# Optimization experiments

Measured on AMD Instinct MI355X. Metric: run time of the kernel, lower is better.

The kernel has to match this reference:

```python
import jax, jax.numpy as jnp
import numpy as np

B, LO, LQ = 4, 2048, 2048
NIN, H, G, NH = 41, 128, 10, 2


def _lin(key, din, dout):
    kw, kb = jax.random.split(key)
    W = jax.random.normal(kw, (din, dout), jnp.float32) / np.float32(np.sqrt(din))
    b = jax.random.normal(kb, (dout,), jnp.float32) * 0.01
    return W, b


def setup_inputs() -> dict:
    key = jax.random.key(0)
    ks = jax.random.split(key, 24)
    t_obs = jax.random.normal(ks[0], (B, LO, 1), jnp.float32)
    ch_obs = jax.random.randint(ks[1], (B, LO, 1), 0, NIN).astype(jnp.float32)
    v_obs = jax.random.normal(ks[2], (B, LO, 1), jnp.float32)
    obs = jnp.concatenate([t_obs, ch_obs, v_obs], -1)  # [B, LO, 3]
    t_q = jax.random.normal(ks[3], (B, LQ, 1), jnp.float32)
    ch_q = jax.random.randint(ks[4], (B, LQ, 1), 0, NIN).astype(jnp.float32)
    xq = jnp.concatenate([t_q, ch_q], -1)  # [B, LQ, 2]
    mobs = (jax.random.uniform(ks[5], (B, LO)) < 0.9).astype(jnp.float32)
    mq = (jax.random.uniform(ks[6], (B, LQ)) < 0.9).astype(jnp.float32)
    w_q0, b_q0 = _lin(ks[7], 1, 1)
    w_q1, b_q1 = _lin(ks[8], 1, H - 1)
    w_o0, b_o0 = _lin(ks[9], 1, 1)
    w_o1, b_o1 = _lin(ks[10], 1, H - 1)
    w_cobs, b_cobs = _lin(ks[11], NIN, H)
    w_cq, b_cq = _lin(ks[12], NIN, H)
    w_qp, b_qp = _lin(ks[13], 2 * H, H)
    w_kp, b_kp = _lin(ks[14], 2 * H + 1, H)
    ws_q, ws_qb = _lin(ks[15], H, H * NH)
    ws_o, ws_ob = _lin(ks[16], H * NH, H)
    ww_q, ww_qb = _lin(ks[17], H, H * NH)
    ww_o, ww_ob = _lin(ks[18], H * NH, H)
    wc_q, wc_qb = _lin(ks[19], H, H * NH)
    wc_o, wc_ob = _lin(ks[20], H * NH, H)
    w_split, b_split = _lin(ks[21], H, H * G)
    mix_wt = jax.random.normal(ks[22], (G, H), jnp.float32)
    w_mix, b_mix = _lin(ks[23], H, 1)
    return dict(obs=obs, mobs=mobs, xq=xq, mq=mq,
                w_q0=w_q0, b_q0=b_q0, w_q1=w_q1, b_q1=b_q1,
                w_o0=w_o0, b_o0=b_o0, w_o1=w_o1, b_o1=b_o1,
                w_cobs=w_cobs, b_cobs=b_cobs, w_cq=w_cq, b_cq=b_cq,
                w_qp=w_qp, b_qp=b_qp, w_kp=w_kp, b_kp=b_kp,
                ws_q=ws_q, ws_qb=ws_qb, ws_o=ws_o, ws_ob=ws_ob,
                ww_q=ww_q, ww_qb=ww_qb, ww_o=ww_o, ww_ob=ww_ob,
                wc_q=wc_q, wc_qb=wc_qb, wc_o=wc_o, wc_ob=wc_ob,
                w_split=w_split, b_split=b_split,
                mix_wt=mix_wt, w_mix=w_mix, b_mix=b_mix)


def _mha(q_in, k_in, v_in, mask, Wq, bq, Wo, bo):
    # Faithful to original: query_param projects q, k AND v (key/val params are unused).
    Bb, Lq, _ = q_in.shape
    Lk = k_in.shape[1]
    q = (q_in @ Wq + bq).reshape(Bb, Lq, NH, H)
    k = (k_in @ Wq + bq).reshape(Bb, Lk, NH, H)
    v = (v_in @ Wq + bq).reshape(Bb, Lk, NH, H)
    scores = jnp.einsum('bqhd,bkhd->bhqk', q, k) / np.float32(np.sqrt(H))
    scores = jnp.where(mask[:, None, :, :] == 0, jnp.float32(-1e6), scores)
    attn = jax.nn.softmax(scores, axis=-1)
    out = jnp.einsum('bhqk,bkhd->bqhd', attn, v).reshape(Bb, Lq, NH * H)
    return q_in + out @ Wo + bo


def _forward(obs, mobs, xq, mq,
             w_q0, b_q0, w_q1, b_q1, w_o0, b_o0, w_o1, b_o1,
             w_cobs, b_cobs, w_cq, b_cq, w_qp, b_qp, w_kp, b_kp,
             ws_q, ws_qb, ws_o, ws_ob, ww_q, ww_qb, ww_o, ww_ob,
             wc_q, wc_qb, wc_o, wc_ob, w_split, b_split,
             mix_wt, w_mix, b_mix):
    cq = xq[:, :, 1]
    tq = xq[:, :, 0:1]
    cobs = obs[:, :, 1]
    tobs = obs[:, :, 0:1]
    xobs = obs[:, :, 2:]
    tq = jnp.concatenate([tq @ w_q0 + b_q0, jnp.sin(tq @ w_q1 + b_q1)], -1)        # [B, LQ, H]
    tobs = jnp.concatenate([tobs @ w_o0 + b_o0, jnp.sin(tobs @ w_o1 + b_o1)], -1)  # [B, LO, H]
    cobs = jax.nn.one_hot(cobs.astype(jnp.int32), NIN, dtype=obs.dtype)
    cq = jax.nn.one_hot(cq.astype(jnp.int32), NIN, dtype=obs.dtype)
    cobs = jax.nn.relu(cobs @ w_cobs + b_cobs)
    cq = jax.nn.relu(cq @ w_cq + b_cq)
    obs_ = jnp.concatenate([tobs, cobs, xobs], -1) * mobs[:, :, None]  # [B, LO, 2H+1]
    xq_ = jnp.concatenate([tq, cq], -1) * mq[:, :, None]               # [B, LQ, 2H]
    qry_embed = xq_ @ w_qp + b_qp    # [B, LQ, H]
    obs_embed = obs_ @ w_kp + b_kp   # [B, LO, H]
    mask_self = mobs[:, :, None] * mobs[:, None, :]   # [B, LO, LO]
    mask_cross = mq[:, :, None] * mobs[:, None, :]    # [B, LQ, LO]
    mask_wts = jnp.broadcast_to(mobs[:, None, :], (obs.shape[0], G, mobs.shape[1]))  # [B, G, LO]
    wts_query = jnp.broadcast_to(mix_wt[None], (obs.shape[0], G, H))
    x = jax.nn.relu(_mha(obs_embed, obs_embed, obs_embed, mask_self, ws_q, ws_qb, ws_o, ws_ob))
    mw_ = _mha(wts_query, x, x, mask_wts, ww_q, ww_qb, ww_o, ww_ob)
    mw = jax.nn.softmax((mw_ @ w_mix + b_mix)[..., 0], axis=-1)  # [B, G]
    x = jax.nn.relu(_mha(qry_embed, x, x, mask_cross, wc_q, wc_qb, wc_o, wc_ob))
    x = (x @ w_split + b_split).reshape(x.shape[0], x.shape[1], G, H)
    return jnp.transpose(x, (0, 2, 1, 3)), mw  # ([B, G, LQ, H], [B, G])


def reference(obs, mobs, xq, mq,
              w_q0, b_q0, w_q1, b_q1, w_o0, b_o0, w_o1, b_o1,
              w_cobs, b_cobs, w_cq, b_cq, w_qp, b_qp, w_kp, b_kp,
              ws_q, ws_qb, ws_o, ws_ob, ww_q, ww_qb, ww_o, ww_ob,
              wc_q, wc_qb, wc_o, wc_ob, w_split, b_split,
              mix_wt, w_mix, b_mix):
    return _forward(obs, mobs, xq, mq,
                    w_q0, b_q0, w_q1, b_q1, w_o0, b_o0, w_o1, b_o1,
                    w_cobs, b_cobs, w_cq, b_cq, w_qp, b_qp, w_kp, b_kp,
                    ws_q, ws_qb, ws_o, ws_ob, ww_q, ww_qb, ww_o, ww_ob,
                    wc_q, wc_qb, wc_o, wc_ob, w_split, b_split,
                    mix_wt, w_mix, b_mix)
```

## Files before the change

kernel.cpp:

```cpp
#include <hip/hip_runtime.h>
#include <hip/hip_bf16.h>

#define B_  4
#define L_  2048
#define H_  128
#define NH_ 2
#define G_  10
#define NIN_ 41

typedef __hip_bfloat16 bf16;
typedef __attribute__((ext_vector_type(8))) short bf16x8s;
typedef __attribute__((ext_vector_type(4))) float f32x4;

__device__ __forceinline__ unsigned short f2bf_bits(float x) {
    __hip_bfloat16 h = __float2bfloat16(x);
    return *reinterpret_cast<unsigned short*>(&h);
}
__device__ __forceinline__ float us2f(unsigned short s) {
    return __uint_as_float(((unsigned int)s) << 16);
}

__global__ __launch_bounds__(128)
void featq_kernel(const float* __restrict__ xq, const float* __restrict__ mq,
                  const float* __restrict__ w_q0, const float* __restrict__ b_q0,
                  const float* __restrict__ w_q1, const float* __restrict__ b_q1,
                  const float* __restrict__ w_cq, const float* __restrict__ b_cq,
                  bf16* __restrict__ featq)
{
    const int row = blockIdx.x;
    const int j   = threadIdx.x;
    const float t   = xq[row * 2 + 0];
    const float chf = xq[row * 2 + 1];
    int ch = (int)chf; ch = max(0, min(NIN_ - 1, ch));
    const float m   = mq[row];
    float tf;
    if (j == 0) tf = t * w_q0[0] + b_q0[0];
    else        tf = __sinf(t * w_q1[j - 1] + b_q1[j - 1]);
    float cf = fmaxf(w_cq[ch * H_ + j] + b_cq[j], 0.f);
    featq[(size_t)row * 256 + j]       = __float2bfloat16(tf * m);
    featq[(size_t)row * 256 + 128 + j] = __float2bfloat16(cf * m);
}

__global__ __launch_bounds__(128)
void feato_kernel(const float* __restrict__ obs, const float* __restrict__ mobs,
                  const float* __restrict__ w_o0, const float* __restrict__ b_o0,
                  const float* __restrict__ w_o1, const float* __restrict__ b_o1,
                  const float* __restrict__ w_cobs, const float* __restrict__ b_cobs,
                  bf16* __restrict__ feato)
{
    const int row = blockIdx.x;
    const int j   = threadIdx.x;
    const float t   = obs[row * 3 + 0];
    const float chf = obs[row * 3 + 1];
    const float xv  = obs[row * 3 + 2];
    int ch = (int)chf; ch = max(0, min(NIN_ - 1, ch));
    const float m   = mobs[row];
    float tf;
    if (j == 0) tf = t * w_o0[0] + b_o0[0];
    else        tf = __sinf(t * w_o1[j - 1] + b_o1[j - 1]);
    float cf = fmaxf(w_cobs[ch * H_ + j] + b_cobs[j], 0.f);
    bf16* r = feato + (size_t)row * 288;
    r[j]       = __float2bfloat16(tf * m);
    r[128 + j] = __float2bfloat16(cf * m);
    if (j == 0) r[256] = __float2bfloat16(xv * m);
    if (j < 31) r[257 + j] = __float2bfloat16(0.f);
}

struct WtArgs {
    const float* W[8];
    bf16* T[8];
    int K[8], Kp[8], N[8];
};
__global__ __launch_bounds__(288)
void wtrans_all_kernel(WtArgs a)
{
    const int i = blockIdx.y, n = blockIdx.x, k = threadIdx.x;
    if (n >= a.N[i] || k >= a.Kp[i]) return;
    a.T[i][(size_t)n * a.Kp[i] + k] =
        (k < a.K[i]) ? __float2bfloat16(a.W[i][(size_t)k * a.N[i] + n])
                     : __float2bfloat16(0.f);
}

__global__ __launch_bounds__(256)
void kvtrans_kernel(const bf16* __restrict__ in, bf16* __restrict__ out)
{
    __shared__ unsigned short tile[64 * 136];
    const int tid = threadIdx.x;
    const int l0 = blockIdx.x * 64;
    const int bh = blockIdx.y;
    const unsigned short* src = (const unsigned short*)(in + (size_t)bh * L_ * H_);
    unsigned short* dst = (unsigned short*)(out + (size_t)bh * H_ * L_);
    #pragma unroll
    for (int p = 0; p < 4; p++) {
        const int l = p * 16 + (tid >> 4);
        const int d0 = (tid & 15) * 8;
        *(uint4*)&tile[l * 136 + d0] = *(const uint4*)&src[(size_t)(l0 + l) * H_ + d0];
    }
    __syncthreads();
// ... 27 lines not shown
        bf16x8s af = *(const bf16x8s*)(arow + kc + quad * 8);
        #pragma unroll
        for (int c = 0; c < 4; c++) {
            bf16x8s wf = *(const bf16x8s*)(WT + (size_t)(n0 + c * 16 + l15) * K + kc + quad * 8);
            acc[c] = __builtin_amdgcn_mfma_f32_16x16x32_bf16(af, wf, acc[c], 0, 0, 0);
        }
    }

    #pragma unroll
    for (int c = 0; c < 4; c++) {
        const int n = n0 + c * 16 + l15;
        const float bv = bias[n];
        #pragma unroll
        for (int r = 0; r < 4; r++) {
            const int m = m0 + quad * 4 + r;
            float v = acc[c][r] + bv;
            if (R != nullptr) v += __bfloat162float(R[(size_t)m * N + n]);
            if (do_relu) v = fmaxf(v, 0.f);
            if (mode == 0) {
                ((float*)out)[(size_t)m * N + n] = v;
            } else if (mode == 1) {
                ((bf16*)out)[(size_t)m * N + n] = __float2bfloat16(v);
            } else if (mode == 2) {
                const int b = m >> 11, l = m & 2047, hh = n >> 7, d = n & 127;
                ((bf16*)out)[(((size_t)(b * NH_ + hh)) * L_ + l) * H_ + d] = __float2bfloat16(v);
            } else {
                const int b = m >> 11, q = m & 2047, g = n >> 7, hh = n & 127;
                ((float*)out)[(((size_t)(b * G_ + g)) * L_ + q) * H_ + hh] = v;
            }
        }
    }
}

#define KT_S 136
#define VT_S 72
#define PS_S 72

__global__ __launch_bounds__(512, 2)
void flash_attn_kernel(const bf16* __restrict__ Qb, const bf16* __restrict__ KVb,
                       const bf16* __restrict__ KVTb,
                       const float* __restrict__ mQ, const float* __restrict__ mK,
                       bf16* __restrict__ O)
{
    __shared__ __align__(16) char smem[90112];
    unsigned short* Ks = (unsigned short*)smem;
    unsigned short* Vs = (unsigned short*)(smem + 34816);
    unsigned short* Ps = (unsigned short*)(smem + 71680);
    float* Ocomb = (float*)smem;
    float* mcomb = (float*)(smem + 33792);
    float* lcomb = (float*)(smem + 34048);

    const int tid  = threadIdx.x;
    const int lane = tid & 63;
    const int wave = tid >> 6;
    const int half = wave >> 2;
    const int wq   = wave & 3;
    const int quad = lane >> 4;
    const int l15  = lane & 15;
    const int t256 = tid & 255;
    const int bh = blockIdx.x, b = bh >> 1, h = bh & 1;
    const int q0 = blockIdx.y * 64;

    const bf16* kvb = KVb  + (size_t)bh * L_ * H_;
    const bf16* kvt = KVTb + (size_t)bh * H_ * L_;
    const float* mkb = mK + b * L_;

    const bf16* qrow = Qb + ((size_t)bh * L_ + q0 + wq * 16 + l15) * H_;
    bf16x8s qf[4];
    #pragma unroll
    for (int kc = 0; kc < 4; kc++)
        qf[kc] = *(const bf16x8s*)(qrow + kc * 32 + quad * 8);

    bool qz[4];
    #pragma unroll
    for (int r = 0; r < 4; r++)
        qz[r] = (mQ != nullptr) && (mQ[b * L_ + q0 + wq * 16 + quad * 4 + r] == 0.f);

    float mo[4], li[4];
    f32x4 Oacc[8];
    #pragma unroll
    for (int r = 0; r < 4; r++) { mo[r] = -1e30f; li[r] = 0.f; }
    #pragma unroll
    for (int c = 0; c < 8; c++) Oacc[c] = (f32x4){0.f, 0.f, 0.f, 0.f};

    const float SCALE = 0.08838834764831845f;
    unsigned short* KsH = Ks + half * 64 * KT_S;
    unsigned short* VsH = Vs + half * 128 * VT_S;
    unsigned short* pw  = Ps + wave * 16 * PS_S;

    const int krow_b = t256 >> 4, kcol = (t256 & 15) * 8;
    const int vrow_b = t256 >> 3, vcol = (t256 & 7) * 8;

    uint4 rk[4], rv[4];
    const int ks0 = half * 1024;

    {
        const int kb = ks0;
        #pragma unroll
        for (int p = 0; p < 4; p++)
            rk[p] = *(const uint4*)(kvb + (size_t)(kb + p * 16 + krow_b) * H_ + kcol);
        #pragma unroll
        for (int p = 0; p < 4; p++)
            rv[p] = *(const uint4*)(kvt + (size_t)(p * 32 + vrow_b) * L_ + kb + vcol);
        #pragma unroll
        for (int p = 0; p < 4; p++)
            *(uint4*)&KsH[(p * 16 + krow_b) * KT_S + kcol] = rk[p];
        #pragma unroll
        for (int p = 0; p < 4; p++)
            *(uint4*)&VsH[(p * 32 + vrow_b) * VT_S + vcol] = rv[p];
    }
    __syncthreads();

    for (int it = 0; it < 16; it++) {
        const int kb = ks0 + it * 64;

        if (it + 1 < 16) {
            const int kn = kb + 64;
            #pragma unroll
            for (int p = 0; p < 4; p++)
                rk[p] = *(const uint4*)(kvb + (size_t)(kn + p * 16 + krow_b) * H_ + kcol);
            #pragma unroll
            for (int p = 0; p < 4; p++)
                rv[p] = *(const uint4*)(kvt + (size_t)(p * 32 + vrow_b) * L_ + kn + vcol);
        }

        float koff[4];
        #pragma unroll
        for (int t = 0; t < 4; t++)
            koff[t] = (mkb[kb + t * 16 + l15] != 0.f) ? 0.f : -1000000.f;

        f32x4 sa[4];
        #pragma unroll
        for (int t = 0; t < 4; t++) sa[t] = (f32x4){0.f, 0.f, 0.f, 0.f};
        #pragma unroll
        for (int t = 0; t < 4; t++)
            #pragma unroll
            for (int kc = 0; kc < 4; kc++) {
                bf16x8s kf = *(const bf16x8s*)&KsH[(t * 16 + l15) * KT_S + kc * 32 + quad * 8];
                sa[t] = __builtin_amdgcn_mfma_f32_16x16x32_bf16(qf[kc], kf, sa[t], 0, 0, 0);
            }

        float s[4][4], mx[4];
        #pragma unroll
        for (int r = 0; r < 4; r++) {
            #pragma unroll
            for (int t = 0; t < 4; t++) {
                const float v = sa[t][r] * SCALE + koff[t];
                s[t][r] = qz[r] ? -1000000.f : v;
            }
            mx[r] = fmaxf(fmaxf(s[0][r], s[1][r]), fmaxf(s[2][r], s[3][r]));
        }
        #pragma unroll
        for (int off = 1; off < 16; off <<= 1)
            #pragma unroll
            for (int r = 0; r < 4; r++) mx[r] = fmaxf(mx[r], __shfl_xor(mx[r], off));

        float al[4], rs[4];
        #pragma unroll
        for (int r = 0; r < 4; r++) {
            const float mn = fmaxf(mo[r], mx[r]);
            al[r] = __expf(mo[r] - mn);
            mo[r] = mn;
            rs[r] = 0.f;
        }
        #pragma unroll
        for (int t = 0; t < 4; t++)
            #pragma unroll
            for (int r = 0; r < 4; r++) {
                const float p = __expf(s[t][r] - mo[r]);
                rs[r] += p;
                pw[(quad * 4 + r) * PS_S + t * 16 + l15] = f2bf_bits(p);
            }
        #pragma unroll
        for (int off = 1; off < 16; off <<= 1)
            #pragma unroll
            for (int r = 0; r < 4; r++) rs[r] += __shfl_xor(rs[r], off);
        #pragma unroll
        for (int r = 0; r < 4; r++) li[r] = li[r] * al[r] + rs[r];
        #pragma unroll
        for (int c = 0; c < 8; c++)
            #pragma unroll
            for (int r = 0; r < 4; r++) Oacc[c][r] *= al[r];

        bf16x8s pf0 = *(bf16x8s*)&pw[l15 * PS_S + quad * 8];
        bf16x8s pf1 = *(bf16x8s*)&pw[l15 * PS_S + 32 + quad * 8];

        #pragma unroll
        for (int c = 0; c < 8; c++) {
            bf16x8s v0 = *(const bf16x8s*)&VsH[(c * 16 + l15) * VT_S + quad * 8];
            bf16x8s v1 = *(const bf16x8s*)&VsH[(c * 16 + l15) * VT_S + 32 + quad * 8];
            Oacc[c] = __builtin_amdgcn_mfma_f32_16x16x32_bf16(pf0, v0, Oacc[c], 0, 0, 0);
            Oacc[c] = __builtin_amdgcn_mfma_f32_16x16x32_bf16(pf1, v1, Oacc[c], 0, 0, 0);
        }

        __syncthreads();
        if (it + 1 < 16) {
            #pragma unroll
            for (int p = 0; p < 4; p++)
                *(uint4*)&KsH[(p * 16 + krow_b) * KT_S + kcol] = rk[p];
            #pragma unroll
            for (int p = 0; p < 4; p++)
                *(uint4*)&VsH[(p * 32 + vrow_b) * VT_S + vcol] = rv[p];
            __syncthreads();
        }
    }

    if (half == 1) {
        #pragma unroll
        for (int c = 0; c < 8; c++)
            #pragma unroll
            for (int r = 0; r < 4; r++)
                Ocomb[(size_t)(wq * 16 + quad * 4 + r) * 132 + c * 16 + l15] = Oacc[c][r];
        if (l15 == 0) {
            #pragma unroll
            for (int r = 0; r < 4; r++) {
                mcomb[wq * 16 + quad * 4 + r] = mo[r];
                lcomb[wq * 16 + quad * 4 + r] = li[r];
            }
        }
    }
    __syncthreads();
    if (half == 0) {
        bf16* orow = O + ((size_t)b * L_ + q0 + wq * 16) * (NH_ * H_) + h * H_;
        #pragma unroll
        for (int r = 0; r < 4; r++) {
            const int row = quad * 4 + r;
            const float m1 = mcomb[wq * 16 + row];
            const float l1 = lcomb[wq * 16 + row];
            const float M  = fmaxf(mo[r], m1);
            const float a0 = __expf(mo[r] - M);
            const float a1 = __expf(m1 - M);
            const float inv = 1.f / (a0 * li[r] + a1 * l1);
            #pragma unroll
            for (int c = 0; c < 8; c++)
                orow[(size_t)row * (NH_ * H_) + c * 16 + l15] =
                    __float2bfloat16((a0 * Oacc[c][r] +
                                      a1 * Ocomb[(size_t)(wq * 16 + row) * 132 + c * 16 + l15]) * inv);
        }
    }
}

__global__ __launch_bounds__(256)
void qmwb_kernel(const float* __restrict__ mixwt, const float* __restrict__ W,
                 const float* __restrict__ bias, bf16* __restrict__ qmwb)
{
    const int g = blockIdx.x;
    const int c = threadIdx.x;
    const int h = c >> 7, d = c & 127;
    if (g >= G_) { qmwb[((size_t)h * 16 + g) * 128 + d] = __float2bfloat16(0.f); return; }
    __shared__ float xr[128];
    if (c < 128) xr[c] = mixwt[g * 128 + c];
    __syncthreads();
    float acc = bias[c];
    #pragma unroll 8
    for (int i = 0; i < 128; i++)
        acc += xr[i] * W[i * 256 + c];
    qmwb[((size_t)h * 16 + g) * 128 + d] = __float2bfloat16(acc);
}

__global__ __launch_bounds__(256)
void mwpartial_kernel(const bf16* __restrict__ qmwb, const bf16* __restrict__ kvmw,
                      const float* __restrict__ mK,
                      float* __restrict__ mwO, float* __restrict__ mwM,
                      float* __restrict__ mwL)
{
    __shared__ __align__(16) unsigned short Ks[128 * 136];
    __shared__ float Qs[10 * 128];
    __shared__ float sc[10 * 128];
    __shared__ float mst[10], lst[10];

// ... 203 lines not shown
    bf16* kvmw  = (bf16*)(ws + 20 * MB + 512 * KB);
    bf16* kvT   = (bf16*)(ws + 24 * MB + 512 * KB);
    char* wbase = ws + 28 * MB + 512 * KB;
    bf16* wqpT  = (bf16*)(wbase + 0);
    bf16* wkpT  = (bf16*)(wbase + 64 * KB);
    bf16* wsqT  = (bf16*)(wbase + 136 * KB);
    bf16* wsoT  = (bf16*)(wbase + 200 * KB);
    bf16* wwqT  = (bf16*)(wbase + 264 * KB);
    bf16* wcqT  = (bf16*)(wbase + 328 * KB);
    bf16* wcoT  = (bf16*)(wbase + 392 * KB);
    bf16* wsplT = (bf16*)(wbase + 456 * KB);
    bf16* qmwb  = (bf16*)(wbase + 776 * KB);
    float* mwO  = (float*)(wbase + 784 * KB);
    float* mwM  = (float*)(wbase + 1424 * KB);
    float* mwL  = (float*)(wbase + 1432 * KB);
    float* mwat = (float*)(wbase + 1440 * KB);
    float* mw_  = (float*)(wbase + 1480 * KB);
    bf16* kvbs  = featq;
    bf16* qcb   = featq;
    bf16* kvcb  = (bf16*)(ws + 4 * MB);
    bf16* abuf2 = abuf;

    WtArgs wa;
    wa.W[0]=w_qp;   wa.T[0]=wqpT;  wa.K[0]=256; wa.Kp[0]=256; wa.N[0]=128;
    wa.W[1]=w_kp;   wa.T[1]=wkpT;  wa.K[1]=257; wa.Kp[1]=288; wa.N[1]=128;
    wa.W[2]=ws_q;   wa.T[2]=wsqT;  wa.K[2]=128; wa.Kp[2]=128; wa.N[2]=256;
    wa.W[3]=ws_o;   wa.T[3]=wsoT;  wa.K[3]=256; wa.Kp[3]=256; wa.N[3]=128;
    wa.W[4]=ww_q;   wa.T[4]=wwqT;  wa.K[4]=128; wa.Kp[4]=128; wa.N[4]=256;
    wa.W[5]=wc_q;   wa.T[5]=wcqT;  wa.K[5]=128; wa.Kp[5]=128; wa.N[5]=256;
    wa.W[6]=wc_o;   wa.T[6]=wcoT;  wa.K[6]=256; wa.Kp[6]=256; wa.N[6]=128;
    wa.W[7]=w_split;wa.T[7]=wsplT; wa.K[7]=128; wa.Kp[7]=128; wa.N[7]=1280;
    wtrans_all_kernel<<<dim3(1280, 8), 288, 0, stream>>>(wa);

    featq_kernel<<<NROW, 128, 0, stream>>>(xq, mq, w_q0, b_q0, w_q1, b_q1,
                                           w_cq, b_cq, featq);
    feato_kernel<<<NROW, 128, 0, stream>>>(obs, mobs, w_o0, b_o0, w_o1, b_o1,
                                           w_cobs, b_cobs, feato);
    gemm_kernel<<<dim3(NROW/32, 2), 128, 0, stream>>>(featq, wqpT, b_qp, nullptr,
                                                      qe_bf, 256, 128, 1, 0);
    gemm_kernel<<<dim3(NROW/32, 2), 128, 0, stream>>>(feato, wkpT, b_kp, nullptr,
                                                      oe_bf, 288, 128, 1, 0);
    gemm_kernel<<<dim3(NROW/32, 4), 128, 0, stream>>>(oe_bf, wsqT, ws_qb, nullptr,
                                                      kvbs, 128, 256, 2, 0);
    kvtrans_kernel<<<dim3(L_/64, B_*NH_), 256, 0, stream>>>(kvbs, kvT);
    flash_attn_kernel<<<dim3(B_*NH_, L_/64), 512, 0, stream>>>(kvbs, kvbs, kvT,
                                                               nullptr, mobs, abuf);
    gemm_kernel<<<dim3(NROW/32, 2), 128, 0, stream>>>(abuf, wsoT, ws_ob, oe_bf,
                                                      x_bf, 256, 128, 1, 1);
    qmwb_kernel<<<16, 256, 0, stream>>>(mix_wt, ww_q, ww_qb, qmwb);
    gemm_kernel<<<dim3(NROW/32, 4), 128, 0, stream>>>(x_bf, wwqT, ww_qb, nullptr,
                                                      kvmw, 128, 256, 2, 0);
    mwpartial_kernel<<<dim3(16, NH_, B_), 256, 0, stream>>>(qmwb, kvmw, mobs,
                                                            mwO, mwM, mwL);
    mwcombine_kernel<<<B_ * G_, 256, 0, stream>>>(mwO, mwM, mwL, mwat);
    mwproj_kernel<<<B_ * G_, 128, 0, stream>>>(mwat, mix_wt, ww_o, ww_ob, mw_);
    mwfinal_kernel<<<B_, 64, 0, stream>>>(mw_, w_mix, b_mix,
                                          out + (size_t)B_ * G_ * L_ * H_);
    gemm_kernel<<<dim3(2*NROW/32, 4), 128, 0, stream>>>(qe_bf, wcqT, wc_qb, nullptr,
                                                        qcb, 128, 256, 2, 0);
    kvtrans_kernel<<<dim3(L_/64, B_*NH_), 256, 0, stream>>>(kvcb, kvT);
    flash_attn_kernel<<<dim3(B_*NH_, L_/64), 512, 0, stream>>>(qcb, kvcb, kvT,
                                                               mq, mobs, abuf2);
    gemm_kernel<<<dim3(NROW/32, 2), 128, 0, stream>>>(abuf2, wcoT, wc_ob, qe_bf,
                                                      x2_bf, 256, 128, 1, 1);
    gemm_kernel<<<dim3(NROW/32, 20), 128, 0, stream>>>(x2_bf, wsplT, b_split, nullptr,
                                                       out, 128, 1280, 3, 0);

    (void)in_sizes; (void)n_in; (void)out_size;
}
```

Measured before the change: 496.0 us.

## Split flash attention keys four ways with two query tiles per wave

The flash attention kernel now splits the key range into four quarters instead of two. Each wave processes two 16-row query tiles against a 32-key block, so each K/V fragment loaded from shared memory feeds two MFMAs. Partial results from the three non-leading quarters are merged through shared memory in a four-way softmax combine. Separately, the two feature-embedding kernels are merged into one launch. The cost is more shared memory (about 100KB per block), which may limit occupancy given launch bounds of 2 blocks, plus more registers.

```diff
diff --git a/kernel.cpp b/kernel.cpp
--- a/kernel.cpp
+++ b/kernel.cpp
@@ -21,49 +21,48 @@
 }
 
 __global__ __launch_bounds__(128)
-void featq_kernel(const float* __restrict__ xq, const float* __restrict__ mq,
-                  const float* __restrict__ w_q0, const float* __restrict__ b_q0,
-                  const float* __restrict__ w_q1, const float* __restrict__ b_q1,
-                  const float* __restrict__ w_cq, const float* __restrict__ b_cq,
-                  bf16* __restrict__ featq)
-{
-    const int row = blockIdx.x;
+void featall_kernel(const float* __restrict__ xq, const float* __restrict__ mq,
+                    const float* __restrict__ obs, const float* __restrict__ mobs,
+                    const float* __restrict__ w_q0, const float* __restrict__ b_q0,
+                    const float* __restrict__ w_q1, const float* __restrict__ b_q1,
+                    const float* __restrict__ w_cq, const float* __restrict__ b_cq,
+                    const float* __restrict__ w_o0, const float* __restrict__ b_o0,
+                    const float* __restrict__ w_o1, const float* __restrict__ b_o1,
+                    const float* __restrict__ w_cobs, const float* __restrict__ b_cobs,
+                    bf16* __restrict__ featq, bf16* __restrict__ feato)
+{
+    const int blk = blockIdx.x;
     const int j   = threadIdx.x;
-    const float t   = xq[row * 2 + 0];
-    const float chf = xq[row * 2 + 1];
-    int ch = (int)chf; ch = max(0, min(NIN_ - 1, ch));
-    const float m   = mq[row];
-    float tf;
-    if (j == 0) tf = t * w_q0[0] + b_q0[0];
-    else        tf = __sinf(t * w_q1[j - 1] + b_q1[j - 1]);
-    float cf = fmaxf(w_cq[ch * H_ + j] + b_cq[j], 0.f);
-    featq[(size_t)row * 256 + j]       = __float2bfloat16(tf * m);
-    featq[(size_t)row * 256 + 128 + j] = __float2bfloat16(cf * m);
-}
-
-__global__ __launch_bounds__(128)
-void feato_kernel(const float* __restrict__ obs, const float* __restrict__ mobs,
-                  const float* __restrict__ w_o0, const float* __restrict__ b_o0,
-                  const float* __restrict__ w_o1, const float* __restrict__ b_o1,
-                  const float* __restrict__ w_cobs, const float* __restrict__ b_cobs,
-                  bf16* __restrict__ feato)
-{
-    const int row = blockIdx.x;
-    const int j   = threadIdx.x;
-    const float t   = obs[row * 3 + 0];
-    const float chf = obs[row * 3 + 1];
-    const float xv  = obs[row * 3 + 2];
-    int ch = (int)chf; ch = max(0, min(NIN_ - 1, ch));
-    const float m   = mobs[row];
-    float tf;
-    if (j == 0) tf = t * w_o0[0] + b_o0[0];
-    else        tf = __sinf(t * w_o1[j - 1] + b_o1[j - 1]);
-    float cf = fmaxf(w_cobs[ch * H_ + j] + b_cobs[j], 0.f);
-    bf16* r = feato + (size_t)row * 288;
-    r[j]       = __float2bfloat16(tf * m);
-    r[128 + j] = __float2bfloat16(cf * m);
-    if (j == 0) r[256] = __float2bfloat16(xv * m);
-    if (j < 31) r[257 + j] = __float2bfloat16(0.f);
+    const int NROW = B_ * L_;
+    if (blk < NROW) {
+        const int row = blk;
+        const float t   = xq[row * 2 + 0];
+        const float chf = xq[row * 2 + 1];
+        int ch = (int)chf; ch = max(0, min(NIN_ - 1, ch));
+        const float m   = mq[row];
+        float tf;
+        if (j == 0) tf = t * w_q0[0] + b_q0[0];
+        else        tf = __sinf(t * w_q1[j - 1] + b_q1[j - 1]);
+        float cf = fmaxf(w_cq[ch * H_ + j] + b_cq[j], 0.f);
+        featq[(size_t)row * 256 + j]       = __float2bfloat16(tf * m);
+        featq[(size_t)row * 256 + 128 + j] = __float2bfloat16(cf * m);
+    } else {
+        const int row = blk - NROW;
+        const float t   = obs[row * 3 + 0];
+        const float chf = obs[row * 3 + 1];
+        const float xv  = obs[row * 3 + 2];
+        int ch = (int)chf; ch = max(0, min(NIN_ - 1, ch));
+        const float m   = mobs[row];
+        float tf;
+        if (j == 0) tf = t * w_o0[0] + b_o0[0];
+        else        tf = __sinf(t * w_o1[j - 1] + b_o1[j - 1]);
+        float cf = fmaxf(w_cobs[ch * H_ + j] + b_cobs[j], 0.f);
+        bf16* r = feato + (size_t)row * 288;
+        r[j]       = __float2bfloat16(tf * m);
+        r[128 + j] = __float2bfloat16(cf * m);
+        if (j == 0) r[256] = __float2bfloat16(xv * m);
+        if (j < 31) r[257 + j] = __float2bfloat16(0.f);
+    }
 }
 
 struct WtArgs {
@@ -158,8 +157,8 @@
 }
 
 #define KT_S 136
-#define VT_S 72
-#define PS_S 72
+#define VT_S 40
+#define PS_S 40
 
 __global__ __launch_bounds__(512, 2)
 void flash_attn_kernel(const bf16* __restrict__ Qb, const bf16* __restrict__ KVb,
@@ -167,200 +166,248 @@
                        const float* __restrict__ mQ, const float* __restrict__ mK,
                        bf16* __restrict__ O)
 {
-    __shared__ __align__(16) char smem[90112];
-    unsigned short* Ks = (unsigned short*)smem;
-    unsigned short* Vs = (unsigned short*)(smem + 34816);
-    unsigned short* Ps = (unsigned short*)(smem + 71680);
-    float* Ocomb = (float*)smem;
-    float* mcomb = (float*)(smem + 33792);
-    float* lcomb = (float*)(smem + 34048);
+    __shared__ __align__(16) char smem[102912];
 
     const int tid  = threadIdx.x;
     const int lane = tid & 63;
     const int wave = tid >> 6;
-    const int half = wave >> 2;
-    const int wq   = wave & 3;
+    const int qtr  = wave >> 1;
+    const int qw   = wave & 1;
     const int quad = lane >> 4;
     const int l15  = lane & 15;
-    const int t256 = tid & 255;
     const int bh = blockIdx.x, b = bh >> 1, h = bh & 1;
     const int q0 = blockIdx.y * 64;
+
+    unsigned short* KsQ = (unsigned short*)(smem + qtr * 8704);
+    unsigned short* VsQ = (unsigned short*)(smem + 34816 + qtr * 10240);
+    unsigned short* pw  = (unsigned short*)(smem + 75776 + wave * 2560);
+    float* Ocomb = (float*)smem;
+    float* mcomb = (float*)(smem + 101376);
+    float* lcomb = (float*)(smem + 102144);
 
     const bf16* kvb = KVb  + (size_t)bh * L_ * H_;
     const bf16* kvt = KVTb + (size_t)bh * H_ * L_;
     const float* mkb = mK + b * L_;
 
-    const bf16* qrow = Qb + ((size_t)bh * L_ + q0 + wq * 16 + l15) * H_;
-    bf16x8s qf[4];
+    bf16x8s qf[2][4];
     #pragma unroll
-    for (int kc = 0; kc < 4; kc++)
-        qf[kc] = *(const bf16x8s*)(qrow + kc * 32 + quad * 8);
-
-    bool qz[4];
+    for (int qt = 0; qt < 2; qt++) {
+        const bf16* qrow = Qb + ((size_t)bh * L_ + q0 + qw * 32 + qt * 16 + l15) * H_;
+        #pragma unroll
+        for (int kc = 0; kc < 4; kc++)
+            qf[qt][kc] = *(const bf16x8s*)(qrow + kc * 32 + quad * 8);
+    }
+
+    bool qz[2][4];
     #pragma unroll
-    for (int r = 0; r < 4; r++)
-        qz[r] = (mQ != nullptr) && (mQ[b * L_ + q0 + wq * 16 + quad * 4 + r] == 0.f);
-
-    float mo[4], li[4];
-    f32x4 Oacc[8];
+    for (int qt = 0; qt < 2; qt++)
+        #pragma unroll
+        for (int r = 0; r < 4; r++)
+            qz[qt][r] = (mQ != nullptr) &&
+                        (mQ[b * L_ + q0 + qw * 32 + qt * 16 + quad * 4 + r] == 0.f);
+
+    float mo[2][4], li[2][4];
+    f32x4 Oacc[2][8];
     #pragma unroll
-    for (int r = 0; r < 4; r++) { mo[r] = -1e30f; li[r] = 0.f; }
-    #pragma unroll
-    for (int c = 0; c < 8; c++) Oacc[c] = (f32x4){0.f, 0.f, 0.f, 0.f};
+    for (int qt = 0; qt < 2; qt++) {
+        #pragma unroll
+        for (int r = 0; r < 4; r++) { mo[qt][r] = -1e30f; li[qt][r] = 0.f; }
+        #pragma unroll
+        for (int c = 0; c < 8; c++) Oacc[qt][c] = (f32x4){0.f, 0.f, 0.f, 0.f};
+    }
 
     const float SCALE = 0.08838834764831845f;
-    unsigned short* KsH = Ks + half * 64 * KT_S;
-    unsigned short* VsH = Vs + half * 128 * VT_S;
-    unsigned short* pw  = Ps + wave * 16 * PS_S;
-
-    const int krow_b = t256 >> 4, kcol = (t256 & 15) * 8;
-    const int vrow_b = t256 >> 3, vcol = (t256 & 7) * 8;
+    const int ks0 = qtr * 512;
+
+    const int t128 = tid & 127;
+    const int krow = t128 >> 4, kchunk = (t128 & 15) * 8;
+    const int vd   = t128;
 
     uint4 rk[4], rv[4];
-    const int ks0 = half * 1024;
 
     {
         const int kb = ks0;
         #pragma unroll
         for (int p = 0; p < 4; p++)
-            rk[p] = *(const uint4*)(kvb + (size_t)(kb + p * 16 + krow_b) * H_ + kcol);
+            rk[p] = *(const uint4*)(kvb + (size_t)(kb + krow + 8 * p) * H_ + kchunk);
+        #pragma unroll
+        for (int c = 0; c < 4; c++)
+            rv[c] = *(const uint4*)(kvt + (size_t)vd * L_ + kb + c * 8);
         #pragma unroll
         for (int p = 0; p < 4; p++)
-            rv[p] = *(const uint4*)(kvt + (size_t)(p * 32 + vrow_b) * L_ + kb + vcol);
-        #pragma unroll
-        for (int p = 0; p < 4; p++)
-            *(uint4*)&KsH[(p * 16 + krow_b) * KT_S + kcol] = rk[p];
-        #pragma unroll
-        for (int p = 0; p < 4; p++)
-            *(uint4*)&VsH[(p * 32 + vrow_b) * VT_S + vcol] = rv[p];
+            *(uint4*)&KsQ[(krow + 8 * p) * KT_S + kchunk] = rk[p];
+        #pragma unroll
+        for (int c = 0; c < 4; c++)
+            *(uint4*)&VsQ[vd * VT_S + c * 8] = rv[c];
     }
     __syncthreads();
 
     for (int it = 0; it < 16; it++) {
-        const int kb = ks0 + it * 64;
+        const int kb = ks0 + it * 32;
 
         if (it + 1 < 16) {
-            const int kn = kb + 64;
+            const int kn = kb + 32;
             #pragma unroll
             for (int p = 0; p < 4; p++)
-                rk[p] = *(const uint4*)(kvb + (size_t)(kn + p * 16 + krow_b) * H_ + kcol);
-            #pragma unroll
-            for (int p = 0; p < 4; p++)
-                rv[p] = *(const uint4*)(kvt + (size_t)(p * 32 + vrow_b) * L_ + kn + vcol);
-        }
-
-        float koff[4];
-        #pragma unroll
-        for (int t = 0; t < 4; t++)
+                rk[p] = *(const uint4*)(kvb + (size_t)(kn + krow + 8 * p) * H_ + kchunk);
+            #pragma unroll
+            for (int c = 0; c < 4; c++)
+                rv[c] = *(const uint4*)(kvt + (size_t)vd * L_ + kn + c * 8);
+        }
+
+        float koff[2];
+        #pragma unroll
+        for (int t = 0; t < 2; t++)
             koff[t] = (mkb[kb + t * 16 + l15] != 0.f) ? 0.f : -1000000.f;
 
-        f32x4 sa[4];
-        #pragma unroll
-        for (int t = 0; t < 4; t++) sa[t] = (f32x4){0.f, 0.f, 0.f, 0.f};
-        #pragma unroll
-        for (int t = 0; t < 4; t++)
+        f32x4 sa[2][2];
+        #pragma unroll
+        for (int qt = 0; qt < 2; qt++)
+            #pragma unroll
+            for (int t = 0; t < 2; t++) sa[qt][t] = (f32x4){0.f, 0.f, 0.f, 0.f};
+        #pragma unroll
+        for (int t = 0; t < 2; t++)
             #pragma unroll
             for (int kc = 0; kc < 4; kc++) {
-                bf16x8s kf = *(const bf16x8s*)&KsH[(t * 16 + l15) * KT_S + kc * 32 + quad * 8];
-                sa[t] = __builtin_amdgcn_mfma_f32_16x16x32_bf16(qf[kc], kf, sa[t], 0, 0, 0);
+                bf16x8s kf = *(const bf16x8s*)&KsQ[(t * 16 + l15) * KT_S + kc * 32 + quad * 8];
+                #pragma unroll
+                for (int qt = 0; qt < 2; qt++)
+                    sa[qt][t] = __builtin_amdgcn_mfma_f32_16x16x32_bf16(qf[qt][kc], kf, sa[qt][t], 0, 0, 0);
             }
 
-        float s[4][4], mx[4];
-        #pragma unroll
-        for (int r = 0; r < 4; r++) {
-            #pragma unroll
-            for (int t = 0; t < 4; t++) {
-                const float v = sa[t][r] * SCALE + koff[t];
-                s[t][r] = qz[r] ? -1000000.f : v;
+        float s[2][2][4], mx[2][4];
+        #pragma unroll
+        for (int qt = 0; qt < 2; qt++)
+            #pragma unroll
+            for (int r = 0; r < 4; r++) {
+                #pragma unroll
+                for (int t = 0; t < 2; t++) {
+                    const float v = sa[qt][t][r] * SCALE + koff[t];
+                    s[qt][t][r] = qz[qt][r] ? -1000000.f : v;
+                }
+                mx[qt][r] = fmaxf(s[qt][0][r], s[qt][1][r]);
             }
-            mx[r] = fmaxf(fmaxf(s[0][r], s[1][r]), fmaxf(s[2][r], s[3][r]));
-        }
         #pragma unroll
         for (int off = 1; off < 16; off <<= 1)
             #pragma unroll
-            for (int r = 0; r < 4; r++) mx[r] = fmaxf(mx[r], __shfl_xor(mx[r], off));
-
-        float al[4], rs[4];
-        #pragma unroll
-        for (int r = 0; r < 4; r++) {
-            const float mn = fmaxf(mo[r], mx[r]);
-            al[r] = __expf(mo[r] - mn);
-            mo[r] = mn;
-            rs[r] = 0.f;
-        }
-        #pragma unroll
-        for (int t = 0; t < 4; t++)
+            for (int qt = 0; qt < 2; qt++)
+                #pragma unroll
+                for (int r = 0; r < 4; r++)
+                    mx[qt][r] = fmaxf(mx[qt][r], __shfl_xor(mx[qt][r], off));
+
+        float al[2][4], rs[2][4];
+        #pragma unroll
+        for (int qt = 0; qt < 2; qt++)
             #pragma unroll
             for (int r = 0; r < 4; r++) {
-                const float p = __expf(s[t][r] - mo[r]);
-                rs[r] += p;
-                pw[(quad * 4 + r) * PS_S + t * 16 + l15] = f2bf_bits(p);
+                const float mn = fmaxf(mo[qt][r], mx[qt][r]);
+                al[qt][r] = __expf(mo[qt][r] - mn);
+                mo[qt][r] = mn;
+                rs[qt][r] = 0.f;
             }
         #pragma unroll
+        for (int qt = 0; qt < 2; qt++)
+            #pragma unroll
+            for (int t = 0; t < 2; t++)
+                #pragma unroll
+                for (int r = 0; r < 4; r++) {
+                    const float p = __expf(s[qt][t][r] - mo[qt][r]);
+                    rs[qt][r] += p;
+                    pw[(qt * 16 + quad * 4 + r) * PS_S + t * 16 + l15] = f2bf_bits(p);
+                }
+        #pragma unroll
         for (int off = 1; off < 16; off <<= 1)
             #pragma unroll
-            for (int r = 0; r < 4; r++) rs[r] += __shfl_xor(rs[r], off);
-        #pragma unroll
-        for (int r = 0; r < 4; r++) li[r] = li[r] * al[r] + rs[r];
-        #pragma unroll
-        for (int c = 0; c < 8; c++)
-            #pragma unroll
-            for (int r = 0; r < 4; r++) Oacc[c][r] *= al[r];
+            for (int qt = 0; qt < 2; qt++)
+                #pragma unroll
+                for (int r = 0; r < 4; r++)
+                    rs[qt][r] += __shfl_xor(rs[qt][r], off);
+        #pragma unroll
+        for (int qt = 0; qt < 2; qt++) {
+            #pragma unroll
+            for (int r = 0; r < 4; r++) li[qt][r] = li[qt][r] * al[qt][r] + rs[qt][r];
+            #pragma unroll
+            for (int c = 0; c < 8; c++)
+                #pragma unroll
+                for (int r = 0; r < 4; r++) Oacc[qt][c][r] *= al[qt][r];
+        }
 
         bf16x8s pf0 = *(bf16x8s*)&pw[l15 * PS_S + quad * 8];
-        bf16x8s pf1 = *(bf16x8s*)&pw[l15 * PS_S + 32 + quad * 8];
+        bf16x8s pf1 = *(bf16x8s*)&pw[(16 + l15) * PS_S + quad * 8];
 
         #pragma unroll
         for (int c = 0; c < 8; c++) {
-            bf16x8s v0 = *(const bf16x8s*)&VsH[(c * 16 + l15) * VT_S + quad * 8];
-            bf16x8s v1 = *(const bf16x8s*)&VsH[(c * 16 + l15) * VT_S + 32 + quad * 8];
-            Oacc[c] = __builtin_amdgcn_mfma_f32_16x16x32_bf16(pf0, v0, Oacc[c], 0, 0, 0);
-            Oacc[c] = __builtin_amdgcn_mfma_f32_16x16x32_bf16(pf1, v1, Oacc[c], 0, 0, 0);
+            bf16x8s vf = *(const bf16x8s*)&VsQ[(c * 16 + l15) * VT_S + quad * 8];
+            Oacc[0][c] = __builtin_amdgcn_mfma_f32_16x16x32_bf16(pf0, vf, Oacc[0][c], 0, 0, 0);
+            Oacc[1][c] = __builtin_amdgcn_mfma_f32_16x16x32_bf16(pf1, vf, Oacc[1][c], 0, 0, 0);
         }
 
         __syncthreads();
         if (it + 1 < 16) {
             #pragma unroll
             for (int p = 0; p < 4; p++)
-                *(uint4*)&KsH[(p * 16 + krow_b) * KT_S + kcol] = rk[p];
-            #pragma unroll
-            for (int p = 0; p < 4; p++)
-                *(uint4*)&VsH[(p * 32 + vrow_b) * VT_S + vcol] = rv[p];
+                *(uint4*)&KsQ[(krow + 8 * p) * KT_S + kchunk] = rk[p];
+            #pragma unroll
+            for (int c = 0; c < 4; c++)
+                *(uint4*)&VsQ[vd * VT_S + c * 8] = rv[c];
             __syncthreads();
         }
     }
 
-    if (half == 1) {
-        #pragma unroll
-        for (int c = 0; c < 8; c++)
-            #pragma unroll
-            for (int r = 0; r < 4; r++)
-                Ocomb[(size_t)(wq * 16 + quad * 4 + r) * 132 + c * 16 + l15] = Oacc[c][r];
-        if (l15 == 0) {
+    if (qtr > 0) {
+        const int sq = qtr - 1;
+        #pragma unroll
+        for (int qt = 0; qt < 2; qt++) {
+            #pragma unroll
+            for (int c = 0; c < 8; c++)
+                #pragma unroll
+                for (int r = 0; r < 4; r++)
+                    Ocomb[(size_t)(sq * 64 + qw * 32 + qt * 16 + quad * 4 + r) * 132 + c * 16 + l15]
+                        = Oacc[qt][c][r];
+            if (l15 == 0) {
+                #pragma unroll
+                for (int r = 0; r < 4; r++) {
+                    mcomb[sq * 64 + qw * 32 + qt * 16 + quad * 4 + r] = mo[qt][r];
+                    lcomb[sq * 64 + qw * 32 + qt * 16 + quad * 4 + r] = li[qt][r];
+                }
+            }
+        }
+    }
+    __syncthreads();
+    if (qtr == 0) {
+        #pragma unroll
+        for (int qt = 0; qt < 2; qt++) {
+            bf16* orow = O + ((size_t)b * L_ + q0 + qw * 32 + qt * 16) * (NH_ * H_) + h * H_;
             #pragma unroll
             for (int r = 0; r < 4; r++) {
-                mcomb[wq * 16 + quad * 4 + r] = mo[r];
-                lcomb[wq * 16 + quad * 4 + r] = li[r];
+                const int row = quad * 4 + r;
+                const int crow = qw * 32 + qt * 16 + row;
+                float M = mo[qt][r];
+                float ms[3], ls[3];
+                #pragma unroll
+                for (int sq = 0; sq < 3; sq++) {
+                    ms[sq] = mcomb[sq * 64 + crow];
+                    ls[sq] = lcomb[sq * 64 + crow];
+                    M = fmaxf(M, ms[sq]);
+                }
+                const float a0 = __expf(mo[qt][r] - M);
+                float lsum = a0 * li[qt][r];
+                float as[3];
+                #pragma unroll
+                for (int sq = 0; sq < 3; sq++) {
+                    as[sq] = __expf(ms[sq] - M);
+                    lsum += as[sq] * ls[sq];
+                }
+                const float inv = 1.f / lsum;
+                #pragma unroll
+                for (int c = 0; c < 8; c++) {
+                    float v = a0 * Oacc[qt][c][r];
+                    #pragma unroll
+                    for (int sq = 0; sq < 3; sq++)
+                        v += as[sq] * Ocomb[(size_t)(sq * 64 + crow) * 132 + c * 16 + l15];
+                    orow[(size_t)row * (NH_ * H_) + c * 16 + l15] = __float2bfloat16(v * inv);
+                }
             }
-        }
-    }
-    __syncthreads();
-    if (half == 0) {
-        bf16* orow = O + ((size_t)b * L_ + q0 + wq * 16) * (NH_ * H_) + h * H_;
-        #pragma unroll
-        for (int r = 0; r < 4; r++) {
-            const int row = quad * 4 + r;
-            const float m1 = mcomb[wq * 16 + row];
-            const float l1 = lcomb[wq * 16 + row];
-            const float M  = fmaxf(mo[r], m1);
-            const float a0 = __expf(mo[r] - M);
-            const float a1 = __expf(m1 - M);
-            const float inv = 1.f / (a0 * li[r] + a1 * l1);
-            #pragma unroll
-            for (int c = 0; c < 8; c++)
-                orow[(size_t)row * (NH_ * H_) + c * 16 + l15] =
-                    __float2bfloat16((a0 * Oacc[c][r] +
-                                      a1 * Ocomb[(size_t)(wq * 16 + row) * 132 + c * 16 + l15]) * inv);
         }
     }
 }
@@ -630,10 +677,10 @@
     wa.W[7]=w_split;wa.T[7]=wsplT; wa.K[7]=128; wa.Kp[7]=128; wa.N[7]=1280;
     wtrans_all_kernel<<<dim3(1280, 8), 288, 0, stream>>>(wa);
 
-    featq_kernel<<<NROW, 128, 0, stream>>>(xq, mq, w_q0, b_q0, w_q1, b_q1,
-                                           w_cq, b_cq, featq);
-    feato_kernel<<<NROW, 128, 0, stream>>>(obs, mobs, w_o0, b_o0, w_o1, b_o1,
-                                           w_cobs, b_cobs, feato);
+    featall_kernel<<<2 * NROW, 128, 0, stream>>>(xq, mq, obs, mobs,
+                                                 w_q0, b_q0, w_q1, b_q1, w_cq, b_cq,
+                                                 w_o0, b_o0, w_o1, b_o1, w_cobs, b_cobs,
+                                                 featq, feato);
     gemm_kernel<<<dim3(NROW/32, 2), 128, 0, stream>>>(featq, wqpT, b_qp, nullptr,
                                                       qe_bf, 256, 128, 1, 0);
     gemm_kernel<<<dim3(NROW/32, 2), 128, 0, stream>>>(feato, wkpT, b_kp, nullptr,
```

Measured after the change: 545.9 us. 10.1% more time.

## Swizzle flash-attention LDS tiles, compute row sums via MFMA, merge feature kernels

Applied to the files above, without the earlier changes.

Replaces the padded shared-memory strides for the K, V and P tiles with XOR-swizzled unpadded layouts. This cuts LDS use from 90112 to 81920 bytes and is meant to avoid bank conflicts. The softmax row sums now come from an extra MFMA against a ones vector instead of a shuffle-reduction chain, and that sum is broadcast from lane 0 of each quad at the end. The two feature-embedding kernels are merged into one launch to save launch overhead. The swizzle indices must match exactly between writes and reads, and the final broadcast adds one shuffle per row.

```diff
diff --git a/kernel.cpp b/kernel.cpp
--- a/kernel.cpp
+++ b/kernel.cpp
@@ -21,49 +21,48 @@
 }
 
 __global__ __launch_bounds__(128)
-void featq_kernel(const float* __restrict__ xq, const float* __restrict__ mq,
-                  const float* __restrict__ w_q0, const float* __restrict__ b_q0,
-                  const float* __restrict__ w_q1, const float* __restrict__ b_q1,
-                  const float* __restrict__ w_cq, const float* __restrict__ b_cq,
-                  bf16* __restrict__ featq)
-{
-    const int row = blockIdx.x;
+void featall_kernel(const float* __restrict__ xq, const float* __restrict__ mq,
+                    const float* __restrict__ obs, const float* __restrict__ mobs,
+                    const float* __restrict__ w_q0, const float* __restrict__ b_q0,
+                    const float* __restrict__ w_q1, const float* __restrict__ b_q1,
+                    const float* __restrict__ w_cq, const float* __restrict__ b_cq,
+                    const float* __restrict__ w_o0, const float* __restrict__ b_o0,
+                    const float* __restrict__ w_o1, const float* __restrict__ b_o1,
+                    const float* __restrict__ w_cobs, const float* __restrict__ b_cobs,
+                    bf16* __restrict__ featq, bf16* __restrict__ feato)
+{
+    const int blk = blockIdx.x;
     const int j   = threadIdx.x;
-    const float t   = xq[row * 2 + 0];
-    const float chf = xq[row * 2 + 1];
-    int ch = (int)chf; ch = max(0, min(NIN_ - 1, ch));
-    const float m   = mq[row];
-    float tf;
-    if (j == 0) tf = t * w_q0[0] + b_q0[0];
-    else        tf = __sinf(t * w_q1[j - 1] + b_q1[j - 1]);
-    float cf = fmaxf(w_cq[ch * H_ + j] + b_cq[j], 0.f);
-    featq[(size_t)row * 256 + j]       = __float2bfloat16(tf * m);
-    featq[(size_t)row * 256 + 128 + j] = __float2bfloat16(cf * m);
-}
-
-__global__ __launch_bounds__(128)
-void feato_kernel(const float* __restrict__ obs, const float* __restrict__ mobs,
-                  const float* __restrict__ w_o0, const float* __restrict__ b_o0,
-                  const float* __restrict__ w_o1, const float* __restrict__ b_o1,
-                  const float* __restrict__ w_cobs, const float* __restrict__ b_cobs,
-                  bf16* __restrict__ feato)
-{
-    const int row = blockIdx.x;
-    const int j   = threadIdx.x;
-    const float t   = obs[row * 3 + 0];
-    const float chf = obs[row * 3 + 1];
-    const float xv  = obs[row * 3 + 2];
-    int ch = (int)chf; ch = max(0, min(NIN_ - 1, ch));
-    const float m   = mobs[row];
-    float tf;
-    if (j == 0) tf = t * w_o0[0] + b_o0[0];
-    else        tf = __sinf(t * w_o1[j - 1] + b_o1[j - 1]);
-    float cf = fmaxf(w_cobs[ch * H_ + j] + b_cobs[j], 0.f);
-    bf16* r = feato + (size_t)row * 288;
-    r[j]       = __float2bfloat16(tf * m);
-    r[128 + j] = __float2bfloat16(cf * m);
-    if (j == 0) r[256] = __float2bfloat16(xv * m);
-    if (j < 31) r[257 + j] = __float2bfloat16(0.f);
+    const int NROW = B_ * L_;
+    if (blk < NROW) {
+        const int row = blk;
+        const float t   = xq[row * 2 + 0];
+        const float chf = xq[row * 2 + 1];
+        int ch = (int)chf; ch = max(0, min(NIN_ - 1, ch));
+        const float m   = mq[row];
+        float tf;
+        if (j == 0) tf = t * w_q0[0] + b_q0[0];
+        else        tf = __sinf(t * w_q1[j - 1] + b_q1[j - 1]);
+        float cf = fmaxf(w_cq[ch * H_ + j] + b_cq[j], 0.f);
+        featq[(size_t)row * 256 + j]       = __float2bfloat16(tf * m);
+        featq[(size_t)row * 256 + 128 + j] = __float2bfloat16(cf * m);
+    } else {
+        const int row = blk - NROW;
+        const float t   = obs[row * 3 + 0];
+        const float chf = obs[row * 3 + 1];
+        const float xv  = obs[row * 3 + 2];
+        int ch = (int)chf; ch = max(0, min(NIN_ - 1, ch));
+        const float m   = mobs[row];
+        float tf;
+        if (j == 0) tf = t * w_o0[0] + b_o0[0];
+        else        tf = __sinf(t * w_o1[j - 1] + b_o1[j - 1]);
+        float cf = fmaxf(w_cobs[ch * H_ + j] + b_cobs[j], 0.f);
+        bf16* r = feato + (size_t)row * 288;
+        r[j]       = __float2bfloat16(tf * m);
+        r[128 + j] = __float2bfloat16(cf * m);
+        if (j == 0) r[256] = __float2bfloat16(xv * m);
+        if (j < 31) r[257 + j] = __float2bfloat16(0.f);
+    }
 }
 
 struct WtArgs {
@@ -157,9 +156,8 @@
     }
 }
 
-#define KT_S 136
-#define VT_S 72
-#define PS_S 72
+#define KSWZ(row, chunk) (((row) << 7) + ((((chunk) ^ ((row) & 7))) << 3))
+#define VSWZ(row, chunk) (((row) << 6) + ((((chunk) ^ ((row) & 7))) << 3))
 
 __global__ __launch_bounds__(512, 2)
 void flash_attn_kernel(const bf16* __restrict__ Qb, const bf16* __restrict__ KVb,
@@ -167,10 +165,10 @@
                        const float* __restrict__ mQ, const float* __restrict__ mK,
                        bf16* __restrict__ O)
 {
-    __shared__ __align__(16) char smem[90112];
+    __shared__ __align__(16) char smem[81920];
     unsigned short* Ks = (unsigned short*)smem;
-    unsigned short* Vs = (unsigned short*)(smem + 34816);
-    unsigned short* Ps = (unsigned short*)(smem + 71680);
+    unsigned short* Vs = (unsigned short*)(smem + 32768);
+    unsigned short* Ps = (unsigned short*)(smem + 65536);
     float* Ocomb = (float*)smem;
     float* mcomb = (float*)(smem + 33792);
     float* lcomb = (float*)(smem + 34048);
@@ -186,6 +184,10 @@
     const int bh = blockIdx.x, b = bh >> 1, h = bh & 1;
     const int q0 = blockIdx.y * 64;
 
+    unsigned short* KsH = Ks + half * 8192;
+    unsigned short* VsH = Vs + half * 8192;
+    unsigned short* pw  = Ps + wave * 1024;
+
     const bf16* kvb = KVb  + (size_t)bh * L_ * H_;
     const bf16* kvt = KVTb + (size_t)bh * H_ * L_;
     const float* mkb = mK + b * L_;
@@ -201,38 +203,41 @@
     for (int r = 0; r < 4; r++)
         qz[r] = (mQ != nullptr) && (mQ[b * L_ + q0 + wq * 16 + quad * 4 + r] == 0.f);
 
-    float mo[4], li[4];
-    f32x4 Oacc[8];
-    #pragma unroll
-    for (int r = 0; r < 4; r++) { mo[r] = -1e30f; li[r] = 0.f; }
+    bf16x8s vones;
+    #pragma unroll
+    for (int e = 0; e < 8; e++)
+        vones[e] = (l15 == 0) ? (short)0x3F80 : (short)0;
+
+    float mo[4];
+    f32x4 Oacc[8], Osum;
+    #pragma unroll
+    for (int r = 0; r < 4; r++) mo[r] = -1e30f;
     #pragma unroll
     for (int c = 0; c < 8; c++) Oacc[c] = (f32x4){0.f, 0.f, 0.f, 0.f};
+    Osum = (f32x4){0.f, 0.f, 0.f, 0.f};
 
     const float SCALE = 0.08838834764831845f;
-    unsigned short* KsH = Ks + half * 64 * KT_S;
-    unsigned short* VsH = Vs + half * 128 * VT_S;
-    unsigned short* pw  = Ps + wave * 16 * PS_S;
-
-    const int krow_b = t256 >> 4, kcol = (t256 & 15) * 8;
-    const int vrow_b = t256 >> 3, vcol = (t256 & 7) * 8;
+    const int ks0 = half * 1024;
+
+    const int krow_b = t256 >> 4, kchk = t256 & 15;
+    const int vrow_b = t256 >> 3, vchk = t256 & 7;
 
     uint4 rk[4], rv[4];
-    const int ks0 = half * 1024;
 
     {
         const int kb = ks0;
         #pragma unroll
         for (int p = 0; p < 4; p++)
-            rk[p] = *(const uint4*)(kvb + (size_t)(kb + p * 16 + krow_b) * H_ + kcol);
+            rk[p] = *(const uint4*)(kvb + (size_t)(kb + p * 16 + krow_b) * H_ + kchk * 8);
         #pragma unroll
         for (int p = 0; p < 4; p++)
-            rv[p] = *(const uint4*)(kvt + (size_t)(p * 32 + vrow_b) * L_ + kb + vcol);
+            rv[p] = *(const uint4*)(kvt + (size_t)(p * 32 + vrow_b) * L_ + kb + vchk * 8);
         #pragma unroll
         for (int p = 0; p < 4; p++)
-            *(uint4*)&KsH[(p * 16 + krow_b) * KT_S + kcol] = rk[p];
+            *(uint4*)&KsH[KSWZ(p * 16 + krow_b, kchk)] = rk[p];
         #pragma unroll
         for (int p = 0; p < 4; p++)
-            *(uint4*)&VsH[(p * 32 + vrow_b) * VT_S + vcol] = rv[p];
+            *(uint4*)&VsH[VSWZ(p * 32 + vrow_b, vchk)] = rv[p];
     }
     __syncthreads();
 
@@ -243,10 +248,10 @@
             const int kn = kb + 64;
             #pragma unroll
             for (int p = 0; p < 4; p++)
-                rk[p] = *(const uint4*)(kvb + (size_t)(kn + p * 16 + krow_b) * H_ + kcol);
+                rk[p] = *(const uint4*)(kvb + (size_t)(kn + p * 16 + krow_b) * H_ + kchk * 8);
             #pragma unroll
             for (int p = 0; p < 4; p++)
-                rv[p] = *(const uint4*)(kvt + (size_t)(p * 32 + vrow_b) * L_ + kn + vcol);
+                rv[p] = *(const uint4*)(kvt + (size_t)(p * 32 + vrow_b) * L_ + kn + vchk * 8);
         }
 
         float koff[4];
@@ -261,7 +266,7 @@
         for (int t = 0; t < 4; t++)
             #pragma unroll
             for (int kc = 0; kc < 4; kc++) {
-                bf16x8s kf = *(const bf16x8s*)&KsH[(t * 16 + l15) * KT_S + kc * 32 + quad * 8];
+                bf16x8s kf = *(const bf16x8s*)&KsH[KSWZ(t * 16 + l15, kc * 4 + quad)];
                 sa[t] = __builtin_amdgcn_mfma_f32_16x16x32_bf16(qf[kc], kf, sa[t], 0, 0, 0);
             }
 
@@ -280,52 +285,48 @@
             #pragma unroll
             for (int r = 0; r < 4; r++) mx[r] = fmaxf(mx[r], __shfl_xor(mx[r], off));
 
-        float al[4], rs[4];
+        float al[4];
         #pragma unroll
         for (int r = 0; r < 4; r++) {
             const float mn = fmaxf(mo[r], mx[r]);
             al[r] = __expf(mo[r] - mn);
             mo[r] = mn;
-            rs[r] = 0.f;
         }
         #pragma unroll
         for (int t = 0; t < 4; t++)
             #pragma unroll
             for (int r = 0; r < 4; r++) {
                 const float p = __expf(s[t][r] - mo[r]);
-                rs[r] += p;
-                pw[(quad * 4 + r) * PS_S + t * 16 + l15] = f2bf_bits(p);
+                pw[VSWZ(quad * 4 + r, 2 * t + (l15 >> 3)) + (l15 & 7)] = f2bf_bits(p);
             }
         #pragma unroll
-        for (int off = 1; off < 16; off <<= 1)
-            #pragma unroll
-            for (int r = 0; r < 4; r++) rs[r] += __shfl_xor(rs[r], off);
-        #pragma unroll
-        for (int r = 0; r < 4; r++) li[r] = li[r] * al[r] + rs[r];
-        #pragma unroll
         for (int c = 0; c < 8; c++)
             #pragma unroll
             for (int r = 0; r < 4; r++) Oacc[c][r] *= al[r];
-
-        bf16x8s pf0 = *(bf16x8s*)&pw[l15 * PS_S + quad * 8];
-        bf16x8s pf1 = *(bf16x8s*)&pw[l15 * PS_S + 32 + quad * 8];
+        #pragma unroll
+        for (int r = 0; r < 4; r++) Osum[r] *= al[r];
+
+        bf16x8s pf0 = *(bf16x8s*)&pw[VSWZ(l15, quad)];
+        bf16x8s pf1 = *(bf16x8s*)&pw[VSWZ(l15, 4 + quad)];
 
         #pragma unroll
         for (int c = 0; c < 8; c++) {
-            bf16x8s v0 = *(const bf16x8s*)&VsH[(c * 16 + l15) * VT_S + quad * 8];
-            bf16x8s v1 = *(const bf16x8s*)&VsH[(c * 16 + l15) * VT_S + 32 + quad * 8];
+            bf16x8s v0 = *(const bf16x8s*)&VsH[VSWZ(c * 16 + l15, quad)];
+            bf16x8s v1 = *(const bf16x8s*)&VsH[VSWZ(c * 16 + l15, 4 + quad)];
             Oacc[c] = __builtin_amdgcn_mfma_f32_16x16x32_bf16(pf0, v0, Oacc[c], 0, 0, 0);
             Oacc[c] = __builtin_amdgcn_mfma_f32_16x16x32_bf16(pf1, v1, Oacc[c], 0, 0, 0);
         }
+        Osum = __builtin_amdgcn_mfma_f32_16x16x32_bf16(pf0, vones, Osum, 0, 0, 0);
+        Osum = __builtin_amdgcn_mfma_f32_16x16x32_bf16(pf1, vones, Osum, 0, 0, 0);
 
         __syncthreads();
         if (it + 1 < 16) {
             #pragma unroll
             for (int p = 0; p < 4; p++)
-                *(uint4*)&KsH[(p * 16 + krow_b) * KT_S + kcol] = rk[p];
+                *(uint4*)&KsH[KSWZ(p * 16 + krow_b, kchk)] = rk[p];
             #pragma unroll
             for (int p = 0; p < 4; p++)
-                *(uint4*)&VsH[(p * 32 + vrow_b) * VT_S + vcol] = rv[p];
+                *(uint4*)&VsH[VSWZ(p * 32 + vrow_b, vchk)] = rv[p];
             __syncthreads();
         }
     }
@@ -340,7 +341,7 @@
             #pragma unroll
             for (int r = 0; r < 4; r++) {
                 mcomb[wq * 16 + quad * 4 + r] = mo[r];
-                lcomb[wq * 16 + quad * 4 + r] = li[r];
+                lcomb[wq * 16 + quad * 4 + r] = Osum[r];
             }
         }
     }
@@ -349,13 +350,14 @@
         bf16* orow = O + ((size_t)b * L_ + q0 + wq * 16) * (NH_ * H_) + h * H_;
         #pragma unroll
         for (int r = 0; r < 4; r++) {
+            const float li0 = __shfl(Osum[r], (lane & 48));
             const int row = quad * 4 + r;
             const float m1 = mcomb[wq * 16 + row];
             const float l1 = lcomb[wq * 16 + row];
             const float M  = fmaxf(mo[r], m1);
             const float a0 = __expf(mo[r] - M);
             const float a1 = __expf(m1 - M);
-            const float inv = 1.f / (a0 * li[r] + a1 * l1);
+            const float inv = 1.f / (a0 * li0 + a1 * l1);
             #pragma unroll
             for (int c = 0; c < 8; c++)
                 orow[(size_t)row * (NH_ * H_) + c * 16 + l15] =
@@ -630,10 +632,10 @@
     wa.W[7]=w_split;wa.T[7]=wsplT; wa.K[7]=128; wa.Kp[7]=128; wa.N[7]=1280;
     wtrans_all_kernel<<<dim3(1280, 8), 288, 0, stream>>>(wa);
 
-    featq_kernel<<<NROW, 128, 0, stream>>>(xq, mq, w_q0, b_q0, w_q1, b_q1,
-                                           w_cq, b_cq, featq);
-    feato_kernel<<<NROW, 128, 0, stream>>>(obs, mobs, w_o0, b_o0, w_o1, b_o1,
-                                           w_cobs, b_cobs, feato);
+    featall_kernel<<<2 * NROW, 128, 0, stream>>>(xq, mq, obs, mobs,
+                                                 w_q0, b_q0, w_q1, b_q1, w_cq, b_cq,
+                                                 w_o0, b_o0, w_o1, b_o1, w_cobs, b_cobs,
+                                                 featq, feato);
     gemm_kernel<<<dim3(NROW/32, 2), 128, 0, stream>>>(featq, wqpT, b_qp, nullptr,
                                                       qe_bf, 256, 128, 1, 0);
     gemm_kernel<<<dim3(NROW/32, 2), 128, 0, stream>>>(feato, wkpT, b_kp, nullptr,
```

After: 538.0 us. 8.5% more time.
